# Kernel optimization log

Hardware: AMD Instinct MI355X
Metric: run time of the kernel (lower is better)

The kernel has to match this reference:

```python
import jax, jax.numpy as jnp
import numpy as np

K, PS, WS, WT = 7, 7, 8, 1
NHEADS, STRIDE0, STRIDE1 = 2, 4, 1


def reflect(idx, n):
    # mirror (no edge repeat) reflection, as in stnls reflect_bounds
    idx = jnp.where(idx < 0, -idx, idx)
    idx = jnp.where(idx >= n, 2 * (n - 1) - idx, idx)
    return idx


def setup_inputs():
    key = jax.random.key(0)
    k0, k1 = jax.random.split(key)
    B, T, C, H, W = 1, 4, 64, 192, 192
    vid0 = jax.random.normal(k0, (B, T, C, H, W), jnp.float32)
    vid1 = jax.random.normal(k1, (B, T, C, H, W), jnp.float32)
    return {"vid0": vid0, "vid1": vid1}


def _search(vid0, vid1):
    B, T, C, H, W = vid0.shape
    m = NHEADS
    cph = C // m
    psh = PS // 2
    nH, nW = H // STRIDE0, W // STRIDE0
    qh = jnp.arange(nH) * STRIDE0  # query centers (stride0 grid)
    qw = jnp.arange(nW) * STRIDE0
    dy = jnp.arange(PS) - psh  # patch offsets
    h0 = reflect(qh[:, None] + dy[None, :], H)  # [nH, ps]
    w0 = reflect(qw[:, None] + dy[None, :], W)  # [nW, ps]
    # query patches: [B,T,m,cph,nH,nW,ps,ps]
    P0 = vid0[:, :, :, h0[:, None, :, None], w0[None, :, None, :]]
    P0 = P0.reshape(B, T, m, cph, nH, nW, PS, PS)

    wsh = (WS - 1) // 2
    doff = (jnp.arange(WS) - wsh) * STRIDE1  # spatial window offsets
    dts = jnp.arange(-WT, WT + 1)  # temporal window offsets
    DT, DI, DJ = jnp.meshgrid(dts, doff, doff, indexing="ij")
    offs = jnp.stack([DT.ravel(), DI.ravel(), DJ.ravel()], -1)  # [L,3]
    tbase = jnp.arange(T)

    def one_offset(off):
        dt, di, dj = off[0], off[1], off[2]
        tmap = jnp.clip(tbase + dt, 0, T - 1)  # clamp temporal window
        h1 = reflect(qh[:, None] + di + dy[None, :], H)
        w1 = reflect(qw[:, None] + dj + dy[None, :], W)
        P1 = vid1[:, tmap][:, :, :, h1[:, None, :, None], w1[None, :, None, :]]
        P1 = P1.reshape(B, T, m, cph, nH, nW, PS, PS)
        # per-head product distance (inner product over patch)
        return jnp.einsum("btmchwyx,btmchwyx->btmhw", P0, P1)

    dists_all = jax.lax.map(one_offset, offs)  # [L,B,T,m,nH,nW]
    L = offs.shape[0]
    Q = T * nH * nW
    dists_all = jnp.transpose(dists_all, (1, 3, 2, 4, 5, 0)).reshape(B, m, Q, L)
    vals, idx = jax.lax.top_k(dists_all, K)  # prod search: descending

    # candidate center coordinates per (offset, query axis)
    tc = jnp.clip(tbase[None, :] + offs[:, 0:1], 0, T - 1)  # [L,T]
    hc = reflect(qh[None, :] + offs[:, 1:2], H)  # [L,nH]
    wc = reflect(qw[None, :] + offs[:, 2:3], W)  # [L,nW]
    idxr = idx.reshape(B, m, T, nH, nW, K)
    tsel = tc[idxr, tbase[None, None, :, None, None, None]]
    hsel = hc[idxr, jnp.arange(nH)[None, None, None, :, None, None]]
    wsel = wc[idxr, jnp.arange(nW)[None, None, None, None, :, None]]
    inds = jnp.stack([tsel, hsel, wsel], -1).reshape(B, m, Q, K, 3)
    return vals, inds.astype(jnp.int32)


def reference(vid0, vid1):
    # returns (dists [B,nheads,Q,k], inds [B,nheads,Q,k,3])
    return _search(vid0, vid1)
```

## Files before the change

### kernel.cpp

```cpp
#include <hip/hip_runtime.h>


#define HH 192
#define WW 192
#define HW (HH * WW)

#define BS_CSTR 282
#define BS_SZ   (32 * BS_CSTR)
#define AS_CSTR 86

__device__ __forceinline__ int reflect_i(int idx, int n) {
    idx = idx < 0 ? -idx : idx;
    idx = idx >= n ? 2 * (n - 1) - idx : idx;
    return idx;
}

template <int CTRL>
__device__ __forceinline__ float dpp_add(float x) {
    int y = __builtin_amdgcn_update_dpp(0, __float_as_int(x), CTRL, 0xf, 0xf, true);
    return x + __int_as_float(y);
}

__device__ __forceinline__ float reduce32(float v) {
    v = dpp_add<0x111>(v);
    v = dpp_add<0x112>(v);
    v = dpp_add<0x114>(v);
    v = dpp_add<0x118>(v);
    v = dpp_add<0x142>(v);
    return v;
}

__global__ __launch_bounds__(256) void nls_kernel(
    const float* __restrict__ vid0,
    const float* __restrict__ vid1,
    float* __restrict__ out)
{
    __shared__ float smem[BS_SZ + 2 * 192];
    float* Bs = smem;
    float* As = smem;
    float* score = smem + BS_SZ;

    const int b    = blockIdx.x;
    const int xcd  = b & 7;
    const int loc  = b >> 3;
    const int qjp  = loc % 24;
    const int r1   = loc / 24;
    const int qi_l = r1 % 6;
    const int r2   = r1 / 6;
    const int t    = r2 & 3;
    const int hd   = r2 >> 2;
    const int qi   = xcd * 6 + qi_l;

    const int qh  = qi * 4;
    const int qw0 = qjp * 8;

    const int tid  = threadIdx.x;
    const int lane = tid & 63;
    const int wid  = tid >> 6;

    const bool intA = (qi >= 1) && (qjp >= 1) && (qjp <= 22);
    const bool intB = (qi >= 2) && (qi <= 46) && (qjp >= 1) && (qjp <= 22);

    if (intA) {
        const int sc = tid & 31;
        const int gg = tid >> 5;
        const float* src = vid0 + (size_t)(t * 64 + hd * 32 + sc) * HW
                         + (qh - 3) * WW + (qw0 - 3);
        float* dstc = As + sc * AS_CSTR;
        for (int it = gg; it < 21; it += 8) {
            int u = it / 3, grp = it - u * 3;
            float4 val = *(const float4*)(src + u * WW + 4 * grp);
            float* dp = dstc + u * 12 + 4 * grp;
            *(float2*)(dp)     = make_float2(val.x, val.y);
            *(float2*)(dp + 2) = make_float2(val.z, val.w);
        }
    } else {
        const int sc = tid >> 3;
        const int vl = tid & 7;
        const float* src = vid0 + (size_t)(t * 64 + hd * 32 + sc) * HW;
        const int wa0 = reflect_i(qw0 - 3 + vl, WW);
        const int wa1 = (vl < 4) ? reflect_i(qw0 + 5 + vl, WW) : 0;
        float* dst = As + sc * AS_CSTR + vl;
        #pragma unroll
        for (int u = 0; u < 7; ++u) {
            int hh = reflect_i(qh - 3 + u, HH);
            const float* rp = src + hh * WW;
            dst[u * 12] = rp[wa0];
            if (vl < 4) dst[u * 12 + 8] = rp[wa1];
        }
    }
    __syncthreads();

    const int c     = lane & 31;
    const int hhalf = lane >> 5;
    const int q     = wid >> 1;
    const int d     = wid & 1;

    float a[7][8];
    {
        const float* Ab = As + c * AS_CSTR + 4 * q;
        #pragma unroll
        for (int y = 0; y < 7; ++y) {
            #pragma unroll
            for (int j = 0; j < 4; ++j)
                *(float2*)&a[y][2 * j] = *(const float2*)(Ab + y * 12 + 2 * j);
        }
    }

    const float* Bc = Bs + c * BS_CSTR + (4 * d) * 20 + 4 * q + 4 * hhalf;

    int tprev = -1;
    for (int dtI = 0; dtI < 3; ++dtI) {
        int tp = t + dtI - 1;
        tp = tp < 0 ? 0 : (tp > 3 ? 3 : tp);

        __syncthreads();

        if (tp == tprev) {
            if (tid < 128) {
                int qq = tid >> 6, o = tid & 63;
                score[qq * 192 + dtI * 64 + o] = score[qq * 192 + (dtI - 1) * 64 + o];
            }
            continue;
        }
        tprev = tp;

        if (intB) {
            const int sc = tid & 31;
            const int gg = tid >> 5;
            const float* src = vid1 + (size_t)(tp * 64 + hd * 32 + sc) * HW
                             + (qh - 6) * WW + (qw0 - 6);
            float* dstc = Bs + sc * BS_CSTR;
            for (int it = gg; it < 70; it += 8) {
                int u = it / 5, grp = it - u * 5;
                float4 val = *(const float4*)(src + u * WW + 4 * grp);
                float* dp = dstc + u * 20 + 4 * grp;
                *(float2*)(dp)     = make_float2(val.x, val.y);
                *(float2*)(dp + 2) = make_float2(val.z, val.w);
            }
        } else {
            const int sc = tid >> 3;
            const int vl = tid & 7;
            const float* src = vid1 + (size_t)(tp * 64 + hd * 32 + sc) * HW;
            const int w0 = reflect_i(qw0 - 6 + vl, WW);
            const int w1 = reflect_i(qw0 + 2 + vl, WW);
            const int w2 = (vl < 4) ? reflect_i(qw0 + 10 + vl, WW) : 0;
            float* dst = Bs + sc * BS_CSTR + vl;
            #pragma unroll
            for (int u = 0; u < 14; ++u) {
                int hh2 = reflect_i(qh - 6 + u, HH);
                const float* rp = src + hh2 * WW;
                dst[u * 20]     = rp[w0];
                dst[u * 20 + 8] = rp[w1];
                if (vl < 4) dst[u * 20 + 16] = rp[w2];
            }
        }
        __syncthreads();

        {
            float acc[16];
            #pragma unroll
            for (int k = 0; k < 16; ++k) acc[k] = 0.f;

            #pragma unroll
            for (int r = 0; r < 10; ++r) {
                float rw[12];
                const float* Br = Bc + r * 20;
                #pragma unroll
                for (int j = 0; j < 6; ++j)
                    *(float2*)&rw[2 * j] = *(const float2*)(Br + 2 * j);
                const int dlo = r > 6 ? r - 6 : 0;
                const int dhi = r < 3 ? r : 3;
                #pragma unroll
                for (int dip = 0; dip < 4; ++dip) {
                    if (dip >= dlo && dip <= dhi) {
                        const int y = r - dip;
                        #pragma unroll
                        for (int djp = 0; djp < 4; ++djp) {
                            #pragma unroll
                            for (int x = 0; x < 7; ++x) {
                                acc[dip * 4 + djp] =
                                    fmaf(a[y][x], rw[djp + x], acc[dip * 4 + djp]);
                            }
                        }
                    }
                }
            }

            #pragma unroll
            for (int k = 0; k < 16; ++k) acc[k] = reduce32(acc[k]);

            if ((lane & 31) == 31) {
                float* sp = &score[q * 192 + dtI * 64 + 4 * hhalf];
                #pragma unroll
                for (int dip = 0; dip < 4; ++dip) {
                    float* dp = sp + (4 * d + dip) * 8;
                    *(float2*)(dp)     = make_float2(acc[dip * 4 + 0], acc[dip * 4 + 1]);
                    *(float2*)(dp + 2) = make_float2(acc[dip * 4 + 2], acc[dip * 4 + 3]);
                }
            }
        }
    }

    __syncthreads();

    if (wid < 2) {
        const int qq = wid;
        const int qj = 2 * qjp + qq;
        float v0 = score[qq * 192 + lane];
        float v1 = score[qq * 192 + 64 + lane];
        float v2 = score[qq * 192 + 128 + lane];
        const int qglob = (t * 48 + qi) * 48 + qj;
        const int vbase = (hd * 9216 + qglob) * 7;
        const int ibase = 129024 + vbase * 3;
        for (int r = 0; r < 7; ++r) {
            float bv = v0; int bi = lane;
            if (v1 > bv) { bv = v1; bi = lane + 64; }
            if (v2 > bv) { bv = v2; bi = lane + 128; }
            #pragma unroll
            for (int m = 1; m <= 32; m <<= 1) {
                float ov = __shfl_xor(bv, m);
                int   oi = __shfl_xor(bi, m);
                if (ov > bv || (ov == bv && oi < bi)) { bv = ov; bi = oi; }
            }
            if (lane == 0) {
                out[vbase + r] = bv;
                int dtSel = bi >> 6;
                int rr    = bi & 63;
                int diSel = (rr >> 3) - 3;
                int djSel = (rr & 7) - 3;
                int ts = t + dtSel - 1;
                ts = ts < 0 ? 0 : (ts > 3 ? 3 : ts);
                int hs = reflect_i(qh + diSel, HH);
                int ws = reflect_i(qj * 4 + djSel, WW);
                float* op = out + ibase + 3 * r;
                op[0] = (float)ts;
                op[1] = (float)hs;
                op[2] = (float)ws;
            }
            if ((bi & 63) == lane) {
                int slot = bi >> 6;
                if (slot == 0)      v0 = -3.4e38f;
                else if (slot == 1) v1 = -3.4e38f;
                else                v2 = -3.4e38f;
            }
        }
    }
}

extern "C" void kernel_launch(void* const* d_in, const int* in_sizes, int n_in,
                              void* d_out, int out_size, void* d_ws, size_t ws_size,
                              hipStream_t stream) {
    const float* vid0 = (const float*)d_in[0];
    const float* vid1 = (const float*)d_in[1];
    float* out = (float*)d_out;
    dim3 grid(9216);
    dim3 block(256);
    hipLaunchKernelGGL(nls_kernel, grid, block, 0, stream, vid0, vid1, out);
}
```

Before: 331.5 us.

## Transpose videos to channel-last in workspace and read patches directly from global

Adds a pre-pass kernel that transposes both videos from CHW to HWC layout in the workspace. A new search kernel then reads the query and candidate patches straight from global memory, with channel as the fastest index, so each warp's 32 channel lanes load coalesced. This removes the LDS staging and the block barriers around it. The cost is an extra full read and write of both videos each call, plus reliance on L1/L2 caching for reuse. The old kernel is kept as a fallback when the workspace is too small.

```diff
diff --git a/kernel.cpp b/kernel.cpp
--- a/kernel.cpp
+++ b/kernel.cpp
@@ -4,10 +4,9 @@
 #define HH 192
 #define WW 192
 #define HW (HH * WW)
-
-#define BS_CSTR 282
-#define BS_SZ   (32 * BS_CSTR)
-#define AS_CSTR 86
+#define TSLICE (192 * 192 * 64)
+#define ROWST  (192 * 64)
+#define TVID   (4 * TSLICE)
 
 __device__ __forceinline__ int reflect_i(int idx, int n) {
     idx = idx < 0 ? -idx : idx;
@@ -30,15 +29,37 @@
     return v;
 }
 
-__global__ __launch_bounds__(256) void nls_kernel(
-    const float* __restrict__ vid0,
-    const float* __restrict__ vid1,
+__global__ __launch_bounds__(256) void transpose_k(
+    const float* __restrict__ v0, const float* __restrict__ v1,
+    float* __restrict__ ws)
+{
+    __shared__ float tile[64 * 65];
+    const int wt  = blockIdx.x;
+    const int h   = blockIdx.y;
+    const int z   = blockIdx.z;
+    const int vid = z >> 2;
+    const int t   = z & 3;
+    const int w0  = wt * 64;
+    const int tid = threadIdx.x;
+    const int a   = tid & 63;
+    const int g   = tid >> 6;
+    const float* src = (vid ? v1 : v0) + (size_t)t * 64 * HW + h * WW + w0;
+    float* dst = ws + (size_t)vid * TVID + ((size_t)(t * 192 + h) * 192 + w0) * 64;
+    #pragma unroll
+    for (int cc = g; cc < 64; cc += 4)
+        tile[cc * 65 + a] = src[(size_t)cc * HW + a];
+    __syncthreads();
+    #pragma unroll
+    for (int ww = g; ww < 64; ww += 4)
+        dst[ww * 64 + a] = tile[a * 65 + ww];
+}
+
+__global__ __launch_bounds__(256) void nls_fast(
+    const float* __restrict__ T0,
+    const float* __restrict__ T1,
     float* __restrict__ out)
 {
-    __shared__ float smem[BS_SZ + 2 * 192];
-    float* Bs = smem;
-    float* As = smem;
-    float* score = smem + BS_SZ;
+    __shared__ float score[2 * 192];
 
     const int b    = blockIdx.x;
     const int xcd  = b & 7;
@@ -58,56 +79,48 @@
     const int lane = tid & 63;
     const int wid  = tid >> 6;
 
-    const bool intA = (qi >= 1) && (qjp >= 1) && (qjp <= 22);
-    const bool intB = (qi >= 2) && (qi <= 46) && (qjp >= 1) && (qjp <= 22);
-
-    if (intA) {
-        const int sc = tid & 31;
-        const int gg = tid >> 5;
-        const float* src = vid0 + (size_t)(t * 64 + hd * 32 + sc) * HW
-                         + (qh - 3) * WW + (qw0 - 3);
-        float* dstc = As + sc * AS_CSTR;
-        for (int it = gg; it < 21; it += 8) {
-            int u = it / 3, grp = it - u * 3;
-            float4 val = *(const float4*)(src + u * WW + 4 * grp);
-            float* dp = dstc + u * 12 + 4 * grp;
-            *(float2*)(dp)     = make_float2(val.x, val.y);
-            *(float2*)(dp + 2) = make_float2(val.z, val.w);
-        }
-    } else {
-        const int sc = tid >> 3;
-        const int vl = tid & 7;
-        const float* src = vid0 + (size_t)(t * 64 + hd * 32 + sc) * HW;
-        const int wa0 = reflect_i(qw0 - 3 + vl, WW);
-        const int wa1 = (vl < 4) ? reflect_i(qw0 + 5 + vl, WW) : 0;
-        float* dst = As + sc * AS_CSTR + vl;
-        #pragma unroll
-        for (int u = 0; u < 7; ++u) {
-            int hh = reflect_i(qh - 3 + u, HH);
-            const float* rp = src + hh * WW;
-            dst[u * 12] = rp[wa0];
-            if (vl < 4) dst[u * 12 + 8] = rp[wa1];
-        }
-    }
-    __syncthreads();
-
     const int c     = lane & 31;
     const int hhalf = lane >> 5;
     const int q     = wid >> 1;
     const int d     = wid & 1;
-
-    float a[7][8];
+    const int cg    = hd * 32 + c;
+    const int qwq   = qw0 + 4 * q;
+
+    float a[7][7];
     {
-        const float* Ab = As + c * AS_CSTR + 4 * q;
         #pragma unroll
         for (int y = 0; y < 7; ++y) {
-            #pragma unroll
-            for (int j = 0; j < 4; ++j)
-                *(float2*)&a[y][2 * j] = *(const float2*)(Ab + y * 12 + 2 * j);
-        }
-    }
-
-    const float* Bc = Bs + c * BS_CSTR + (4 * d) * 20 + 4 * q + 4 * hhalf;
+            const int hv = reflect_i(qh - 3 + y, HH);
+            const float* rp = T0 + (size_t)(t * 192 + hv) * ROWST + cg;
+            #pragma unroll
+            for (int x = 0; x < 7; ++x) {
+                const int wv = reflect_i(qwq - 3 + x, WW);
+                a[y][x] = rp[wv * 64];
+            }
+        }
+    }
+
+    const bool interior = (qi >= 2) && (qi <= 46) && (qjp >= 1) && (qjp <= 22);
+
+#define FMA_BLOCK                                                        \
+    {                                                                    \
+        const int dlo = r > 6 ? r - 6 : 0;                               \
+        const int dhi = r < 3 ? r : 3;                                   \
+        _Pragma("unroll")                                                \
+        for (int dip = 0; dip < 4; ++dip) {                              \
+            if (dip >= dlo && dip <= dhi) {                              \
+                const int y = r - dip;                                   \
+                _Pragma("unroll")                                        \
+                for (int djp = 0; djp < 4; ++djp) {                      \
+                    _Pragma("unroll")                                    \
+                    for (int x = 0; x < 7; ++x) {                        \
+                        acc[dip * 4 + djp] =                             \
+                            fmaf(a[y][x], rw[djp + x], acc[dip * 4 + djp]); \
+                    }                                                    \
+                }                                                        \
+            }                                                            \
+        }                                                                \
+    }
 
     int tprev = -1;
     for (int dtI = 0; dtI < 3; ++dtI) {
@@ -125,82 +138,51 @@
         }
         tprev = tp;
 
-        if (intB) {
-            const int sc = tid & 31;
-            const int gg = tid >> 5;
-            const float* src = vid1 + (size_t)(tp * 64 + hd * 32 + sc) * HW
-                             + (qh - 6) * WW + (qw0 - 6);
-            float* dstc = Bs + sc * BS_CSTR;
-            for (int it = gg; it < 70; it += 8) {
-                int u = it / 5, grp = it - u * 5;
-                float4 val = *(const float4*)(src + u * WW + 4 * grp);
-                float* dp = dstc + u * 20 + 4 * grp;
-                *(float2*)(dp)     = make_float2(val.x, val.y);
-                *(float2*)(dp + 2) = make_float2(val.z, val.w);
+        float acc[16];
+        #pragma unroll
+        for (int k = 0; k < 16; ++k) acc[k] = 0.f;
+
+        if (interior) {
+            const float* P = T1 + (size_t)(tp * 192 + qh - 6 + 4 * d) * ROWST
+                           + (qwq - 6 + 4 * hhalf) * 64 + cg;
+            #pragma unroll
+            for (int r = 0; r < 10; ++r) {
+                const float* pr = P + r * ROWST;
+                float rw[10];
+                #pragma unroll
+                for (int v = 0; v < 10; ++v) rw[v] = pr[v * 64];
+                FMA_BLOCK
             }
         } else {
-            const int sc = tid >> 3;
-            const int vl = tid & 7;
-            const float* src = vid1 + (size_t)(tp * 64 + hd * 32 + sc) * HW;
-            const int w0 = reflect_i(qw0 - 6 + vl, WW);
-            const int w1 = reflect_i(qw0 + 2 + vl, WW);
-            const int w2 = (vl < 4) ? reflect_i(qw0 + 10 + vl, WW) : 0;
-            float* dst = Bs + sc * BS_CSTR + vl;
-            #pragma unroll
-            for (int u = 0; u < 14; ++u) {
-                int hh2 = reflect_i(qh - 6 + u, HH);
-                const float* rp = src + hh2 * WW;
-                dst[u * 20]     = rp[w0];
-                dst[u * 20 + 8] = rp[w1];
-                if (vl < 4) dst[u * 20 + 16] = rp[w2];
-            }
-        }
-        __syncthreads();
-
-        {
-            float acc[16];
-            #pragma unroll
-            for (int k = 0; k < 16; ++k) acc[k] = 0.f;
-
+            int wo[10];
+            #pragma unroll
+            for (int v = 0; v < 10; ++v)
+                wo[v] = reflect_i(qwq - 6 + 4 * hhalf + v, WW) * 64 + cg;
+            const float* Pt = T1 + (size_t)tp * TSLICE;
             #pragma unroll
             for (int r = 0; r < 10; ++r) {
-                float rw[12];
-                const float* Br = Bc + r * 20;
-                #pragma unroll
-                for (int j = 0; j < 6; ++j)
-                    *(float2*)&rw[2 * j] = *(const float2*)(Br + 2 * j);
-                const int dlo = r > 6 ? r - 6 : 0;
-                const int dhi = r < 3 ? r : 3;
-                #pragma unroll
-                for (int dip = 0; dip < 4; ++dip) {
-                    if (dip >= dlo && dip <= dhi) {
-                        const int y = r - dip;
-                        #pragma unroll
-                        for (int djp = 0; djp < 4; ++djp) {
-                            #pragma unroll
-                            for (int x = 0; x < 7; ++x) {
-                                acc[dip * 4 + djp] =
-                                    fmaf(a[y][x], rw[djp + x], acc[dip * 4 + djp]);
-                            }
-                        }
-                    }
-                }
-            }
-
-            #pragma unroll
-            for (int k = 0; k < 16; ++k) acc[k] = reduce32(acc[k]);
-
-            if ((lane & 31) == 31) {
-                float* sp = &score[q * 192 + dtI * 64 + 4 * hhalf];
-                #pragma unroll
-                for (int dip = 0; dip < 4; ++dip) {
-                    float* dp = sp + (4 * d + dip) * 8;
-                    *(float2*)(dp)     = make_float2(acc[dip * 4 + 0], acc[dip * 4 + 1]);
-                    *(float2*)(dp + 2) = make_float2(acc[dip * 4 + 2], acc[dip * 4 + 3]);
-                }
-            }
-        }
-    }
+                const int hv = reflect_i(qh - 6 + 4 * d + r, HH);
+                const float* pr = Pt + (size_t)hv * ROWST;
+                float rw[10];
+                #pragma unroll
+                for (int v = 0; v < 10; ++v) rw[v] = pr[wo[v]];
+                FMA_BLOCK
+            }
+        }
+
+        #pragma unroll
+        for (int k = 0; k < 16; ++k) acc[k] = reduce32(acc[k]);
+
+        if ((lane & 31) == 31) {
+            float* sp = &score[q * 192 + dtI * 64 + 4 * hhalf];
+            #pragma unroll
+            for (int dip = 0; dip < 4; ++dip)
+                #pragma unroll
+                for (int djp = 0; djp < 4; ++djp)
+                    sp[(4 * d + dip) * 8 + djp] = acc[dip * 4 + djp];
+        }
+    }
+#undef FMA_BLOCK
 
     __syncthreads();
 
@@ -248,13 +230,233 @@
     }
 }
 
+#define BS_CSTR 282
+#define BS_SZ   (32 * BS_CSTR)
+#define AS_CSTR 86
+
+__global__ __launch_bounds__(256) void nls_kernel(
+    const float* __restrict__ vid0,
+    const float* __restrict__ vid1,
+    float* __restrict__ out)
+{
+    __shared__ float smem[BS_SZ + 2 * 192];
+    float* Bs = smem;
+    float* As = smem;
+    float* score = smem + BS_SZ;
+
+    const int b    = blockIdx.x;
+    const int xcd  = b & 7;
+    const int loc  = b >> 3;
+    const int qjp  = loc % 24;
+    const int r1   = loc / 24;
+    const int qi_l = r1 % 6;
+    const int r2   = r1 / 6;
+    const int t    = r2 & 3;
+    const int hd   = r2 >> 2;
+    const int qi   = xcd * 6 + qi_l;
+
+    const int qh  = qi * 4;
+    const int qw0 = qjp * 8;
+
+    const int tid  = threadIdx.x;
+    const int lane = tid & 63;
+    const int wid  = tid >> 6;
+
+    const bool intA = (qi >= 1) && (qjp >= 1) && (qjp <= 22);
+    const bool intB = (qi >= 2) && (qi <= 46) && (qjp >= 1) && (qjp <= 22);
+
+    if (intA) {
+        const int sc = tid & 31;
+        const int gg = tid >> 5;
+        const float* src = vid0 + (size_t)(t * 64 + hd * 32 + sc) * HW
+                         + (qh - 3) * WW + (qw0 - 3);
+        float* dstc = As + sc * AS_CSTR;
+        for (int it = gg; it < 21; it += 8) {
+            int u = it / 3, grp = it - u * 3;
+            float4 val = *(const float4*)(src + u * WW + 4 * grp);
+            float* dp = dstc + u * 12 + 4 * grp;
+            *(float2*)(dp)     = make_float2(val.x, val.y);
+            *(float2*)(dp + 2) = make_float2(val.z, val.w);
+        }
+    } else {
+        const int sc = tid >> 3;
+        const int vl = tid & 7;
+        const float* src = vid0 + (size_t)(t * 64 + hd * 32 + sc) * HW;
+        const int wa0 = reflect_i(qw0 - 3 + vl, WW);
+        const int wa1 = (vl < 4) ? reflect_i(qw0 + 5 + vl, WW) : 0;
+        float* dst = As + sc * AS_CSTR + vl;
+        #pragma unroll
+        for (int u = 0; u < 7; ++u) {
+            int hh = reflect_i(qh - 3 + u, HH);
+            const float* rp = src + hh * WW;
+            dst[u * 12] = rp[wa0];
+            if (vl < 4) dst[u * 12 + 8] = rp[wa1];
+        }
+    }
+    __syncthreads();
+
+    const int c     = lane & 31;
+    const int hhalf = lane >> 5;
+    const int q     = wid >> 1;
+    const int d     = wid & 1;
+
+    float a[7][8];
+    {
+        const float* Ab = As + c * AS_CSTR + 4 * q;
+        #pragma unroll
+        for (int y = 0; y < 7; ++y) {
+            #pragma unroll
+            for (int j = 0; j < 4; ++j)
+                *(float2*)&a[y][2 * j] = *(const float2*)(Ab + y * 12 + 2 * j);
+        }
+    }
+
+    const float* Bc = Bs + c * BS_CSTR + (4 * d) * 20 + 4 * q + 4 * hhalf;
+
+    int tprev = -1;
+    for (int dtI = 0; dtI < 3; ++dtI) {
+        int tp = t + dtI - 1;
+        tp = tp < 0 ? 0 : (tp > 3 ? 3 : tp);
+        __syncthreads();
+        if (tp == tprev) {
+            if (tid < 128) {
+                int qq = tid >> 6, o = tid & 63;
+                score[qq * 192 + dtI * 64 + o] = score[qq * 192 + (dtI - 1) * 64 + o];
+            }
+            continue;
+        }
+        tprev = tp;
+
+        if (intB) {
+            const int sc = tid & 31;
+            const int gg = tid >> 5;
+            const float* src = vid1 + (size_t)(tp * 64 + hd * 32 + sc) * HW
+                             + (qh - 6) * WW + (qw0 - 6);
+            float* dstc = Bs + sc * BS_CSTR;
+            for (int it = gg; it < 70; it += 8) {
+                int u = it / 5, grp = it - u * 5;
+                float4 val = *(const float4*)(src + u * WW + 4 * grp);
+                float* dp = dstc + u * 20 + 4 * grp;
+                *(float2*)(dp)     = make_float2(val.x, val.y);
+                *(float2*)(dp + 2) = make_float2(val.z, val.w);
+            }
+        } else {
+            const int sc = tid >> 3;
+            const int vl = tid & 7;
+            const float* src = vid1 + (size_t)(tp * 64 + hd * 32 + sc) * HW;
+            const int w0 = reflect_i(qw0 - 6 + vl, WW);
+            const int w1 = reflect_i(qw0 + 2 + vl, WW);
+            const int w2 = (vl < 4) ? reflect_i(qw0 + 10 + vl, WW) : 0;
+            float* dst = Bs + sc * BS_CSTR + vl;
+            #pragma unroll
+            for (int u = 0; u < 14; ++u) {
+                int hh2 = reflect_i(qh - 6 + u, HH);
+                const float* rp = src + hh2 * WW;
+                dst[u * 20]     = rp[w0];
+                dst[u * 20 + 8] = rp[w1];
+                if (vl < 4) dst[u * 20 + 16] = rp[w2];
+            }
+        }
+        __syncthreads();
+
+        {
+            float acc[16];
+            #pragma unroll
+            for (int k = 0; k < 16; ++k) acc[k] = 0.f;
+            #pragma unroll
+            for (int r = 0; r < 10; ++r) {
+                float rw[12];
+                const float* Br = Bc + r * 20;
+                #pragma unroll
+                for (int j = 0; j < 6; ++j)
+                    *(float2*)&rw[2 * j] = *(const float2*)(Br + 2 * j);
+                const int dlo = r > 6 ? r - 6 : 0;
+                const int dhi = r < 3 ? r : 3;
+                #pragma unroll
+                for (int dip = 0; dip < 4; ++dip) {
+                    if (dip >= dlo && dip <= dhi) {
+                        const int y = r - dip;
+                        #pragma unroll
+                        for (int djp = 0; djp < 4; ++djp)
+                            #pragma unroll
+                            for (int x = 0; x < 7; ++x)
+                                acc[dip * 4 + djp] =
+                                    fmaf(a[y][x], rw[djp + x], acc[dip * 4 + djp]);
+                    }
+                }
+            }
+            #pragma unroll
+            for (int k = 0; k < 16; ++k) acc[k] = reduce32(acc[k]);
+            if ((lane & 31) == 31) {
+                float* sp = &score[q * 192 + dtI * 64 + 4 * hhalf];
+                #pragma unroll
+                for (int dip = 0; dip < 4; ++dip) {
+                    float* dp = sp + (4 * d + dip) * 8;
+                    *(float2*)(dp)     = make_float2(acc[dip * 4 + 0], acc[dip * 4 + 1]);
+                    *(float2*)(dp + 2) = make_float2(acc[dip * 4 + 2], acc[dip * 4 + 3]);
+                }
+            }
+        }
+    }
+
+    __syncthreads();
+
+    if (wid < 2) {
+        const int qq = wid;
+        const int qj = 2 * qjp + qq;
+        float v0 = score[qq * 192 + lane];
+        float v1 = score[qq * 192 + 64 + lane];
+        float v2 = score[qq * 192 + 128 + lane];
+        const int qglob = (t * 48 + qi) * 48 + qj;
+        const int vbase = (hd * 9216 + qglob) * 7;
+        const int ibase = 129024 + vbase * 3;
+        for (int r = 0; r < 7; ++r) {
+            float bv = v0; int bi = lane;
+            if (v1 > bv) { bv = v1; bi = lane + 64; }
+            if (v2 > bv) { bv = v2; bi = lane + 128; }
+            #pragma unroll
+            for (int m = 1; m <= 32; m <<= 1) {
+                float ov = __shfl_xor(bv, m);
+                int   oi = __shfl_xor(bi, m);
+                if (ov > bv || (ov == bv && oi < bi)) { bv = ov; bi = oi; }
+            }
+            if (lane == 0) {
+                out[vbase + r] = bv;
+                int dtSel = bi >> 6;
+                int rr    = bi & 63;
+                int diSel = (rr >> 3) - 3;
+                int djSel = (rr & 7) - 3;
+                int ts = t + dtSel - 1;
+                ts = ts < 0 ? 0 : (ts > 3 ? 3 : ts);
+                int hs = reflect_i(qh + diSel, HH);
+                int ws = reflect_i(qj * 4 + djSel, WW);
+                float* op = out + ibase + 3 * r;
+                op[0] = (float)ts;
+                op[1] = (float)hs;
+                op[2] = (float)ws;
+            }
+            if ((bi & 63) == lane) {
+                int slot = bi >> 6;
+                if (slot == 0)      v0 = -3.4e38f;
+                else if (slot == 1) v1 = -3.4e38f;
+                else                v2 = -3.4e38f;
+            }
+        }
+    }
+}
+
 extern "C" void kernel_launch(void* const* d_in, const int* in_sizes, int n_in,
                               void* d_out, int out_size, void* d_ws, size_t ws_size,
                               hipStream_t stream) {
     const float* vid0 = (const float*)d_in[0];
     const float* vid1 = (const float*)d_in[1];
     float* out = (float*)d_out;
-    dim3 grid(9216);
-    dim3 block(256);
-    hipLaunchKernelGGL(nls_kernel, grid, block, 0, stream, vid0, vid1, out);
-}
+    const size_t need = 2ull * (size_t)TVID * sizeof(float);
+    if (ws_size >= need) {
+        float* ws = (float*)d_ws;
+        transpose_k<<<dim3(3, 192, 8), 256, 0, stream>>>(vid0, vid1, ws);
+        nls_fast<<<dim3(9216), 256, 0, stream>>>(ws, ws + TVID, out);
+    } else {
+        nls_kernel<<<dim3(9216), 256, 0, stream>>>(vid0, vid1, out);
+    }
+}
```

Measured after the change: 339.6 us. 2.5% more time.
